# Performance work log

Measured on AMD Instinct MI355X. Metric: run time of the kernel, lower is better.

The kernel has to match this reference:

```python
import jax, jax.numpy as jnp
import numpy as np

STEP = 1  # spatial shift amount (module hard-codes narrow offset 1, so step=1)
EPS = 1e-5  # BatchNorm eps (torch default)


def conv1x1(x, W, b):
    # x: [B,C,H,W], W: [Co,C], b: [Co]
    return jnp.einsum('bchw,oc->bohw', x, W) + b[None, :, None, None]


def setup_inputs() -> dict:
    key = jax.random.key(0)
    ks = jax.random.split(key, 16)
    B, C, H, W = 32, 160, 112, 112
    Co = C // 5
    d = {}
    d['x'] = jax.random.normal(ks[0], (B, C, H, W), dtype=jnp.float32)
    # BatchNorm (inference-style) params
    d['gamma'] = jax.random.uniform(ks[1], (C,), minval=0.8, maxval=1.2)
    d['beta'] = jax.random.normal(ks[2], (C,)) * 0.05
    d['running_mean'] = jax.random.normal(ks[3], (C,)) * 0.1
    d['running_var'] = jax.random.uniform(ks[4], (C,), minval=0.5, maxval=1.5)
    # five 1x1 branch convs: weight [Co, C], bias [Co]
    names = ['t', 'b', 'r', 'l', 'c']
    for i, n in enumerate(names):
        d[f'W_{n}'] = jax.random.normal(ks[5 + i], (Co, C)) * 0.05
        d[f'b_{n}'] = jnp.zeros((Co,), dtype=jnp.float32)
    # final fuse conv: [C, C]
    d['W_fuse'] = jax.random.normal(ks[10], (C, C)) * 0.05
    d['b_fuse'] = jnp.zeros((C,), dtype=jnp.float32)
    return d


def reference(x, gamma, beta, running_mean, running_var,
              W_t, b_t, W_b, b_b, W_r, b_r, W_l, b_l, W_c, b_c,
              W_fuse, b_fuse):
    B, C, H, Wd = x.shape
    # BatchNorm2d (inference) + exact GELU (torch default)
    inv = gamma / jnp.sqrt(running_var + EPS)
    h = (x - running_mean[None, :, None, None]) * inv[None, :, None, None] + beta[None, :, None, None]
    h = jax.nn.gelu(h, approximate=False)
    # five parallel 1x1 projections, each C -> C//5
    xt = conv1x1(h, W_t, b_t)
    xb = conv1x1(h, W_b, b_b)
    xr = conv1x1(h, W_r, b_r)
    xl = conv1x1(h, W_l, b_l)
    xc = conv1x1(h, W_c, b_c)
    # spatial shifts: pad + narrow (torch F.pad order is (left,right,top,bottom))
    # x_t: pad bottom by STEP, take rows [1, 1+H)  -> shift up
    xt = jnp.pad(xt, ((0, 0), (0, 0), (0, STEP), (0, 0)))[:, :, 1:1 + H, :]
    # x_b: pad top by STEP, take rows [0, H)       -> shift down
    xb = jnp.pad(xb, ((0, 0), (0, 0), (STEP, 0), (0, 0)))[:, :, :H, :]
    # x_l: pad right by STEP, take cols [1, 1+W)   -> shift left
    xl = jnp.pad(xl, ((0, 0), (0, 0), (0, 0), (0, STEP)))[:, :, :, 1:1 + Wd]
    # x_r: pad left by STEP, take cols [0, W)      -> shift right
    xr = jnp.pad(xr, ((0, 0), (0, 0), (0, 0), (STEP, 0)))[:, :, :, :Wd]
    # concat in original order [t, b, r, l, c] then final 1x1 fuse
    cat = jnp.concatenate([xt, xb, xr, xl, xc], axis=1)  # [B, C, H, W]
    return conv1x1(cat, W_fuse, b_fuse)
```

## Files before the change

kernel.cpp:

```cpp
#include <hip/hip_runtime.h>
#include <hip/hip_bf16.h>

#define BATCH 32
#define C 160
#define H 112
#define W 112
#define HW (H * W)
#define NT 7
#define HP (H / 2)

typedef __bf16 bf16_t;
typedef bf16_t bf16x8 __attribute__((ext_vector_type(8)));
typedef float f32x4 __attribute__((ext_vector_type(4)));

#define P_BYTES   ((size_t)BATCH * C * HW * 2)
#define WALL_OFF  (P_BYTES)
#define WFRAG_B   (10 * 5 * 64 * 8 * 2)
#define WFUSE_OFF (WALL_OFF + WFRAG_B)
#define BN2_OFF   (WFUSE_OFF + WFRAG_B)
#define BALL_OFF  (BN2_OFF + C * 8)

__device__ __forceinline__ float gelu_exact(float h) {
    float u  = h * 0.70710678118654752f;
    float au = __builtin_fabsf(u);
    float tt = __builtin_amdgcn_rcpf(__builtin_fmaf(0.3275911f, au, 1.0f));
    float poly = tt * __builtin_fmaf(tt,
                      __builtin_fmaf(tt,
                      __builtin_fmaf(tt,
                      __builtin_fmaf(tt, 1.061405429f, -1.453152027f),
                                         1.421413741f),
                                        -0.284496736f),
                                         0.254829592f);
    float e  = __builtin_amdgcn_exp2f(-au * au * 1.4426950408889634f);
    float er = __builtin_fmaf(-poly, e, 1.0f);
    er = __builtin_copysignf(er, u);
    return 0.5f * h * (1.0f + er);
}

__global__ __launch_bounds__(256) void prep_kernel(
    const float* __restrict__ Wt, const float* __restrict__ Wb,
    const float* __restrict__ Wr, const float* __restrict__ Wl,
    const float* __restrict__ Wc,
    const float* __restrict__ bt, const float* __restrict__ bb,
    const float* __restrict__ br, const float* __restrict__ bl,
    const float* __restrict__ bc,
    const float* __restrict__ Wfuse,
    const float* __restrict__ gamma, const float* __restrict__ beta,
    const float* __restrict__ mean, const float* __restrict__ var,
    char* __restrict__ ws)
{
    bf16_t* wallf  = (bf16_t*)(ws + WALL_OFF);
    bf16_t* wfusef = (bf16_t*)(ws + WFUSE_OFF);
    float2* bn2 = (float2*)(ws + BN2_OFF);
    float*  ball = (float*)(ws + BALL_OFF);

    const float* Wbr[5] = {Wt, Wb, Wr, Wl, Wc};
    const float* bbr[5] = {bt, bb, br, bl, bc};

    int tid = blockIdx.x * blockDim.x + threadIdx.x;
    int nth = gridDim.x * blockDim.x;

    for (int idx = tid; idx < 10 * 5 * 64 * 8; idx += nth) {
        int j    = idx & 7;
        int lane = (idx >> 3) & 63;
        int rest = idx >> 9;
        int ks   = rest % 5;
        int mt   = rest / 5;
        int m  = mt * 16 + (lane & 15);
        int q  = lane >> 4;
        int k_nat = ks * 32 + q * 8 + j;
        wallf[idx] = (bf16_t)Wbr[m >> 5][(m & 31) * C + k_nat];
        int chan32 = (j < 4) ? (q * 4 + j) : (16 + q * 4 + (j - 4));
        wfusef[idx] = (bf16_t)Wfuse[m * C + ks * 32 + chan32];
    }
    for (int c = tid; c < C; c += nth) {
        float s = gamma[c] * rsqrtf(var[c] + 1e-5f);
        bn2[c] = make_float2(s, beta[c] - mean[c] * s);
        ball[c] = bbr[c >> 5][c & 31];
    }
}

__global__ __launch_bounds__(256, 2) void stage1_kernel(
    const float* __restrict__ x, char* __restrict__ ws)
{
    const bf16_t* __restrict__ wallf = (const bf16_t*)(ws + WALL_OFF);
    const float2* __restrict__ bn2 = (const float2*)(ws + BN2_OFF);
    const float*  __restrict__ ball = (const float*)(ws + BALL_OFF);
    bf16_t* __restrict__ P = (bf16_t*)ws;

    int wid  = blockIdx.x * 4 + (threadIdx.x >> 6);
    int lane = threadIdx.x & 63;
    int b   = wid / (HP * NT);
    int rem = wid - b * (HP * NT);
    int yp  = rem / NT;
    int t   = rem - yp * NT;
    int y0  = yp * 2;
    int nl = lane & 15, quad = lane >> 4;
    int px = t * 16 + nl;

    const float* xp = x + (size_t)b * C * HW + (size_t)y0 * W + px;

    float v0[40], v1[40];
#pragma unroll
    for (int i = 0; i < 40; ++i) {
        int ks = i >> 3, j = i & 7;
        size_t off = (size_t)(ks * 32 + quad * 8 + j) * HW;
        v0[i] = xp[off];
        v1[i] = xp[off + W];
    }
    __builtin_amdgcn_sched_barrier(0);

    f32x4 acc0[10], acc1[10];
#pragma unroll
    for (int mt = 0; mt < 10; ++mt) {
        f32x4 bias = *(const f32x4*)&ball[mt * 16 + quad * 4];
        acc0[mt] = bias;
        acc1[mt] = bias;
    }

#pragma unroll
    for (int ks = 0; ks < 5; ++ks) {
        bf16x8 bfrag0, bfrag1;
#pragma unroll
        for (int j = 0; j < 8; ++j) {
            int c = ks * 32 + quad * 8 + j;
            float2 sb = bn2[c];
            bfrag0[j] = (bf16_t)gelu_exact(__builtin_fmaf(v0[ks * 8 + j], sb.x, sb.y));
            bfrag1[j] = (bf16_t)gelu_exact(__builtin_fmaf(v1[ks * 8 + j], sb.x, sb.y));
        }
#pragma unroll
        for (int mt = 0; mt < 10; ++mt) {
            bf16x8 afrag = *(const bf16x8*)&wallf[((mt * 5 + ks) * 64 + lane) * 8];
            acc0[mt] = __builtin_amdgcn_mfma_f32_16x16x32_bf16(afrag, bfrag0, acc0[mt], 0, 0, 0);
            acc1[mt] = __builtin_amdgcn_mfma_f32_16x16x32_bf16(afrag, bfrag1, acc1[mt], 0, 0, 0);
        }
    }

    size_t pb = (((size_t)(b * 5) * H + y0) * W + px) * 32 + quad * 8;
#pragma unroll
    for (int kb = 0; kb < 5; ++kb) {
        bf16x8 o0, o1;
#pragma unroll
        for (int r = 0; r < 4; ++r) {
            o0[r]     = (bf16_t)acc0[kb * 2][r];
            o0[r + 4] = (bf16_t)acc0[kb * 2 + 1][r];
            o1[r]     = (bf16_t)acc1[kb * 2][r];
            o1[r + 4] = (bf16_t)acc1[kb * 2 + 1][r];
        }
        *(bf16x8*)&P[pb + (size_t)kb * HW * 32] = o0;
        *(bf16x8*)&P[pb + (size_t)kb * HW * 32 + (size_t)W * 32] = o1;
    }
}

__global__ __launch_bounds__(256, 2) void stage2_kernel(
    char* __restrict__ ws, const float* __restrict__ bfuse,
    float* __restrict__ out)
{
    const bf16_t* __restrict__ wfusef = (const bf16_t*)(ws + WFUSE_OFF);
    const bf16_t* __restrict__ P = (const bf16_t*)ws;

    int wid  = blockIdx.x * 4 + (threadIdx.x >> 6);
    int lane = threadIdx.x & 63;
    int b   = wid / (HP * NT);
    int rem = wid - b * (HP * NT);
    int yp  = rem / NT;
    int t   = rem - yp * NT;
    int y0  = yp * 2, y1 = y0 + 1;
    int nl = lane & 15, quad = lane >> 4;
    int px = t * 16 + nl;

    bf16x8 zero;
#pragma unroll
    for (int j = 0; j < 8; ++j) zero[j] = (bf16_t)0.0f;

    auto ldP = [&](int kb, int yy, int xx) -> bf16x8 {
        return *(const bf16x8*)&P[(((size_t)(b * 5 + kb) * H + yy) * W + xx) * 32 + quad * 8];
    };

    bf16x8 f0[5], f1[5];
    f0[0] = ldP(0, y0 + 1, px);
    f0[1] = ldP(1, y0 - 1 < 0 ? 0 : y0 - 1, px);
    f0[2] = ldP(2, y0, px == 0 ? 0 : px - 1);
    f0[3] = ldP(3, y0, px == W - 1 ? px : px + 1);
    f0[4] = ldP(4, y0, px);
    f1[0] = ldP(0, y1 + 1 >= H ? y1 : y1 + 1, px);
    f1[1] = ldP(1, y1 - 1, px);
    f1[2] = ldP(2, y1, px == 0 ? 0 : px - 1);
    f1[3] = ldP(3, y1, px == W - 1 ? px : px + 1);
    f1[4] = ldP(4, y1, px);
    __builtin_amdgcn_sched_barrier(0);

    if (y0 == 0)     f0[1] = zero;
    if (y1 + 1 >= H) f1[0] = zero;
    if (px == 0)     { f0[2] = zero; f1[2] = zero; }
    if (px == W - 1) { f0[3] = zero; f1[3] = zero; }

    f32x4 acc0[10], acc1[10];
#pragma unroll
    for (int mt = 0; mt < 10; ++mt) {
        f32x4 bias = *(const f32x4*)&bfuse[mt * 16 + quad * 4];
        acc0[mt] = bias;
        acc1[mt] = bias;
    }

#pragma unroll
    for (int ks = 0; ks < 5; ++ks) {
#pragma unroll
        for (int mt = 0; mt < 10; ++mt) {
            bf16x8 afrag = *(const bf16x8*)&wfusef[((mt * 5 + ks) * 64 + lane) * 8];
            acc0[mt] = __builtin_amdgcn_mfma_f32_16x16x32_bf16(afrag, f0[ks], acc0[mt], 0, 0, 0);
            acc1[mt] = __builtin_amdgcn_mfma_f32_16x16x32_bf16(afrag, f1[ks], acc1[mt], 0, 0, 0);
        }
    }

    size_t ob = (size_t)b * C * HW + (size_t)y0 * W + px;
#pragma unroll
    for (int mt = 0; mt < 10; ++mt) {
#pragma unroll
        for (int r = 0; r < 4; ++r) {
            int m = mt * 16 + quad * 4 + r;
            out[ob + (size_t)m * HW] = acc0[mt][r];
            out[ob + (size_t)m * HW + W] = acc1[mt][r];
        }
    }
}

extern "C" void kernel_launch(void* const* d_in, const int* in_sizes, int n_in,
                              void* d_out, int out_size, void* d_ws, size_t ws_size,
                              hipStream_t stream)
{
    const float* x     = (const float*)d_in[0];
    const float* gamma = (const float*)d_in[1];
    const float* beta  = (const float*)d_in[2];
    const float* mean  = (const float*)d_in[3];
    const float* var   = (const float*)d_in[4];
    const float* Wt    = (const float*)d_in[5];
    const float* bt    = (const float*)d_in[6];
    const float* Wb    = (const float*)d_in[7];
    const float* bb    = (const float*)d_in[8];
    const float* Wr    = (const float*)d_in[9];
    const float* br    = (const float*)d_in[10];
    const float* Wl    = (const float*)d_in[11];
    const float* bl    = (const float*)d_in[12];
    const float* Wc    = (const float*)d_in[13];
    const float* bc    = (const float*)d_in[14];
    const float* Wfuse = (const float*)d_in[15];
    const float* bfuse = (const float*)d_in[16];

    char* ws = (char*)d_ws;
    float* out = (float*)d_out;

    prep_kernel<<<64, 256, 0, stream>>>(Wt, Wb, Wr, Wl, Wc, bt, bb, br, bl, bc,
                                        Wfuse, gamma, beta, mean, var, ws);

    int nblocks = (BATCH * HP * NT) / 4;
    stage1_kernel<<<nblocks, 256, 0, stream>>>(x, ws);
    stage2_kernel<<<nblocks, 256, 0, stream>>>(ws, bfuse, out);
}
```

Before: 590.1 us.

## Fold branch convs into fuse weights and apply shifts on GELU activations

New measurement: 928.8 us. 57.4% more time.

```diff
diff --git a/kernel.cpp b/kernel.cpp
--- a/kernel.cpp
+++ b/kernel.cpp
@@ -13,12 +13,12 @@
 typedef bf16_t bf16x8 __attribute__((ext_vector_type(8)));
 typedef float f32x4 __attribute__((ext_vector_type(4)));
 
-#define P_BYTES   ((size_t)BATCH * C * HW * 2)
-#define WALL_OFF  (P_BYTES)
-#define WFRAG_B   (10 * 5 * 64 * 8 * 2)
-#define WFUSE_OFF (WALL_OFF + WFRAG_B)
-#define BN2_OFF   (WFUSE_OFF + WFRAG_B)
-#define BALL_OFF  (BN2_OFF + C * 8)
+#define H_BYTES   ((size_t)BATCH * HW * C * 2)
+#define WTAP_OFF  (H_BYTES)
+#define WTAP_B    (5 * C * C * 2)
+#define BTOT_OFF  (WTAP_OFF + WTAP_B)
+#define BIASK_OFF (BTOT_OFF + 640)
+#define BN2_OFF   (BIASK_OFF + 3200)
 
 __device__ __forceinline__ float gelu_exact(float h) {
     float u  = h * 0.70710678118654752f;
@@ -44,15 +44,15 @@
     const float* __restrict__ bt, const float* __restrict__ bb,
     const float* __restrict__ br, const float* __restrict__ bl,
     const float* __restrict__ bc,
-    const float* __restrict__ Wfuse,
+    const float* __restrict__ Wfuse, const float* __restrict__ bfuse,
     const float* __restrict__ gamma, const float* __restrict__ beta,
     const float* __restrict__ mean, const float* __restrict__ var,
     char* __restrict__ ws)
 {
-    bf16_t* wallf  = (bf16_t*)(ws + WALL_OFF);
-    bf16_t* wfusef = (bf16_t*)(ws + WFUSE_OFF);
-    float2* bn2 = (float2*)(ws + BN2_OFF);
-    float*  ball = (float*)(ws + BALL_OFF);
+    bf16_t* wtapf = (bf16_t*)(ws + WTAP_OFF);
+    float*  btot  = (float*)(ws + BTOT_OFF);
+    float*  biask = (float*)(ws + BIASK_OFF);
+    float2* bn2   = (float2*)(ws + BN2_OFF);
 
     const float* Wbr[5] = {Wt, Wb, Wr, Wl, Wc};
     const float* bbr[5] = {bt, bb, br, bl, bc};
@@ -60,104 +60,83 @@
     int tid = blockIdx.x * blockDim.x + threadIdx.x;
     int nth = gridDim.x * blockDim.x;
 
-    for (int idx = tid; idx < 10 * 5 * 64 * 8; idx += nth) {
+    for (int idx = tid; idx < 5 * 10 * 5 * 64 * 8; idx += nth) {
         int j    = idx & 7;
         int lane = (idx >> 3) & 63;
         int rest = idx >> 9;
-        int ks   = rest % 5;
-        int mt   = rest / 5;
-        int m  = mt * 16 + (lane & 15);
-        int q  = lane >> 4;
-        int k_nat = ks * 32 + q * 8 + j;
-        wallf[idx] = (bf16_t)Wbr[m >> 5][(m & 31) * C + k_nat];
-        int chan32 = (j < 4) ? (q * 4 + j) : (16 + q * 4 + (j - 4));
-        wfusef[idx] = (bf16_t)Wfuse[m * C + ks * 32 + chan32];
+        int kb   = rest % 5;
+        int tmp  = rest / 5;
+        int ks   = tmp % 5;
+        int mt   = tmp / 5;
+        int m = mt * 16 + (lane & 15);
+        int k = ks * 32 + (lane >> 4) * 8 + j;
+        float s = 0.0f;
+        const float* wf = Wfuse + m * C + kb * 32;
+        const float* wb2 = Wbr[kb];
+#pragma unroll 8
+        for (int o = 0; o < 32; ++o)
+            s = __builtin_fmaf(wf[o], wb2[o * C + k], s);
+        wtapf[idx] = (bf16_t)s;
     }
     for (int c = tid; c < C; c += nth) {
-        float s = gamma[c] * rsqrtf(var[c] + 1e-5f);
-        bn2[c] = make_float2(s, beta[c] - mean[c] * s);
-        ball[c] = bbr[c >> 5][c & 31];
-    }
-}
-
-__global__ __launch_bounds__(256, 2) void stage1_kernel(
+        float tot = bfuse[c];
+        for (int kb = 0; kb < 5; ++kb) {
+            float s = 0.0f;
+            const float* wf = Wfuse + c * C + kb * 32;
+            for (int o = 0; o < 32; ++o)
+                s = __builtin_fmaf(wf[o], bbr[kb][o], s);
+            biask[kb * C + c] = s;
+            tot += s;
+        }
+        btot[c] = tot;
+        float sc = gamma[c] * rsqrtf(var[c] + 1e-5f);
+        bn2[c] = make_float2(sc, beta[c] - mean[c] * sc);
+    }
+}
+
+__global__ __launch_bounds__(256) void stageh_kernel(
     const float* __restrict__ x, char* __restrict__ ws)
 {
-    const bf16_t* __restrict__ wallf = (const bf16_t*)(ws + WALL_OFF);
     const float2* __restrict__ bn2 = (const float2*)(ws + BN2_OFF);
-    const float*  __restrict__ ball = (const float*)(ws + BALL_OFF);
-    bf16_t* __restrict__ P = (bf16_t*)ws;
-
-    int wid  = blockIdx.x * 4 + (threadIdx.x >> 6);
-    int lane = threadIdx.x & 63;
-    int b   = wid / (HP * NT);
-    int rem = wid - b * (HP * NT);
-    int yp  = rem / NT;
-    int t   = rem - yp * NT;
-    int y0  = yp * 2;
-    int nl = lane & 15, quad = lane >> 4;
-    int px = t * 16 + nl;
-
-    const float* xp = x + (size_t)b * C * HW + (size_t)y0 * W + px;
-
-    float v0[40], v1[40];
-#pragma unroll
-    for (int i = 0; i < 40; ++i) {
-        int ks = i >> 3, j = i & 7;
-        size_t off = (size_t)(ks * 32 + quad * 8 + j) * HW;
-        v0[i] = xp[off];
-        v1[i] = xp[off + W];
-    }
-    __builtin_amdgcn_sched_barrier(0);
-
-    f32x4 acc0[10], acc1[10];
-#pragma unroll
-    for (int mt = 0; mt < 10; ++mt) {
-        f32x4 bias = *(const f32x4*)&ball[mt * 16 + quad * 4];
-        acc0[mt] = bias;
-        acc1[mt] = bias;
-    }
-
-#pragma unroll
-    for (int ks = 0; ks < 5; ++ks) {
-        bf16x8 bfrag0, bfrag1;
-#pragma unroll
-        for (int j = 0; j < 8; ++j) {
-            int c = ks * 32 + quad * 8 + j;
-            float2 sb = bn2[c];
-            bfrag0[j] = (bf16_t)gelu_exact(__builtin_fmaf(v0[ks * 8 + j], sb.x, sb.y));
-            bfrag1[j] = (bf16_t)gelu_exact(__builtin_fmaf(v1[ks * 8 + j], sb.x, sb.y));
-        }
-#pragma unroll
-        for (int mt = 0; mt < 10; ++mt) {
-            bf16x8 afrag = *(const bf16x8*)&wallf[((mt * 5 + ks) * 64 + lane) * 8];
-            acc0[mt] = __builtin_amdgcn_mfma_f32_16x16x32_bf16(afrag, bfrag0, acc0[mt], 0, 0, 0);
-            acc1[mt] = __builtin_amdgcn_mfma_f32_16x16x32_bf16(afrag, bfrag1, acc1[mt], 0, 0, 0);
-        }
-    }
-
-    size_t pb = (((size_t)(b * 5) * H + y0) * W + px) * 32 + quad * 8;
-#pragma unroll
-    for (int kb = 0; kb < 5; ++kb) {
-        bf16x8 o0, o1;
-#pragma unroll
-        for (int r = 0; r < 4; ++r) {
-            o0[r]     = (bf16_t)acc0[kb * 2][r];
-            o0[r + 4] = (bf16_t)acc0[kb * 2 + 1][r];
-            o1[r]     = (bf16_t)acc1[kb * 2][r];
-            o1[r + 4] = (bf16_t)acc1[kb * 2 + 1][r];
-        }
-        *(bf16x8*)&P[pb + (size_t)kb * HW * 32] = o0;
-        *(bf16x8*)&P[pb + (size_t)kb * HW * 32 + (size_t)W * 32] = o1;
-    }
-}
-
-__global__ __launch_bounds__(256, 2) void stage2_kernel(
-    char* __restrict__ ws, const float* __restrict__ bfuse,
-    float* __restrict__ out)
-{
-    const bf16_t* __restrict__ wfusef = (const bf16_t*)(ws + WFUSE_OFF);
-    const bf16_t* __restrict__ P = (const bf16_t*)ws;
+    bf16_t* __restrict__ h = (bf16_t*)ws;
+
+    int tid = blockIdx.x * 256 + threadIdx.x;
+    int x2  = tid % 56;
+    int y   = (tid / 56) % H;
+    int c32 = (tid / (56 * H)) % 5;
+    int b   = tid / (56 * H * 5);
+    int px  = x2 * 2;
+
+    const float* xp = x + ((size_t)b * C + c32 * 32) * HW + y * W + px;
+
+    float2 v[32];
+#pragma unroll
+    for (int j = 0; j < 32; ++j)
+        v[j] = *(const float2*)(xp + (size_t)j * HW);
+
+    bf16x8 o0[4], o1[4];
+#pragma unroll
+    for (int j = 0; j < 32; ++j) {
+        float2 sb = bn2[c32 * 32 + j];
+        o0[j >> 3][j & 7] = (bf16_t)gelu_exact(__builtin_fmaf(v[j].x, sb.x, sb.y));
+        o1[j >> 3][j & 7] = (bf16_t)gelu_exact(__builtin_fmaf(v[j].y, sb.x, sb.y));
+    }
+
+    bf16_t* hp = h + ((size_t)b * HW + (size_t)y * W + px) * C + c32 * 32;
+#pragma unroll
+    for (int k = 0; k < 4; ++k) {
+        *(bf16x8*)(hp + k * 8) = o0[k];
+        *(bf16x8*)(hp + C + k * 8) = o1[k];
+    }
+}
+
+__global__ __launch_bounds__(256, 2) void stagef_kernel(
+    char* __restrict__ ws, float* __restrict__ out)
+{
+    const bf16_t* __restrict__ h = (const bf16_t*)ws;
+    const bf16_t* __restrict__ wtapf = (const bf16_t*)(ws + WTAP_OFF);
+    const float*  __restrict__ btot  = (const float*)(ws + BTOT_OFF);
+    const float*  __restrict__ biask = (const float*)(ws + BIASK_OFF);
 
     int wid  = blockIdx.x * 4 + (threadIdx.x >> 6);
     int lane = threadIdx.x & 63;
@@ -169,47 +148,91 @@
     int nl = lane & 15, quad = lane >> 4;
     int px = t * 16 + nl;
 
-    bf16x8 zero;
-#pragma unroll
-    for (int j = 0; j < 8; ++j) zero[j] = (bf16_t)0.0f;
-
-    auto ldP = [&](int kb, int yy, int xx) -> bf16x8 {
-        return *(const bf16x8*)&P[(((size_t)(b * 5 + kb) * H + yy) * W + xx) * 32 + quad * 8];
-    };
-
-    bf16x8 f0[5], f1[5];
-    f0[0] = ldP(0, y0 + 1, px);
-    f0[1] = ldP(1, y0 - 1 < 0 ? 0 : y0 - 1, px);
-    f0[2] = ldP(2, y0, px == 0 ? 0 : px - 1);
-    f0[3] = ldP(3, y0, px == W - 1 ? px : px + 1);
-    f0[4] = ldP(4, y0, px);
-    f1[0] = ldP(0, y1 + 1 >= H ? y1 : y1 + 1, px);
-    f1[1] = ldP(1, y1 - 1, px);
-    f1[2] = ldP(2, y1, px == 0 ? 0 : px - 1);
-    f1[3] = ldP(3, y1, px == W - 1 ? px : px + 1);
-    f1[4] = ldP(4, y1, px);
-    __builtin_amdgcn_sched_barrier(0);
-
-    if (y0 == 0)     f0[1] = zero;
-    if (y1 + 1 >= H) f1[0] = zero;
-    if (px == 0)     { f0[2] = zero; f1[2] = zero; }
-    if (px == W - 1) { f0[3] = zero; f1[3] = zero; }
+    bool m_up = (y0 == 0);
+    bool m_dn = (y1 == H - 1);
+    bool m_l  = (px == 0);
+    bool m_r  = (px == W - 1);
+    int ym  = m_up ? 0 : y0 - 1;
+    int ypl = m_dn ? y1 : y1 + 1;
+    int pxl = m_l ? px : px - 1;
+    int pxr = m_r ? px : px + 1;
+
+    const bf16_t* hb = h + (size_t)b * HW * C;
 
     f32x4 acc0[10], acc1[10];
 #pragma unroll
     for (int mt = 0; mt < 10; ++mt) {
-        f32x4 bias = *(const f32x4*)&bfuse[mt * 16 + quad * 4];
+        f32x4 bias = *(const f32x4*)&btot[mt * 16 + quad * 4];
         acc0[mt] = bias;
         acc1[mt] = bias;
     }
 
+    bf16x8 zero;
+#pragma unroll
+    for (int j = 0; j < 8; ++j) zero[j] = (bf16_t)0.0f;
+
 #pragma unroll
     for (int ks = 0; ks < 5; ++ks) {
+        int co = ks * 32 + quad * 8;
+        auto ldh = [&](int yy, int xx) -> bf16x8 {
+            return *(const bf16x8*)&hb[((size_t)yy * W + xx) * C + co];
+        };
+        bf16x8 S0 = ldh(ym, px);
+        bf16x8 S1 = ldh(y0, px);
+        bf16x8 S2 = ldh(y1, px);
+        bf16x8 S3 = ldh(ypl, px);
+        bf16x8 L0 = ldh(y0, pxl);
+        bf16x8 L1 = ldh(y1, pxl);
+        bf16x8 R0 = ldh(y0, pxr);
+        bf16x8 R1 = ldh(y1, pxr);
+        if (m_up) S0 = zero;
+        if (m_dn) S3 = zero;
+        if (m_l) { L0 = zero; L1 = zero; }
+        if (m_r) { R0 = zero; R1 = zero; }
+
 #pragma unroll
         for (int mt = 0; mt < 10; ++mt) {
-            bf16x8 afrag = *(const bf16x8*)&wfusef[((mt * 5 + ks) * 64 + lane) * 8];
-            acc0[mt] = __builtin_amdgcn_mfma_f32_16x16x32_bf16(afrag, f0[ks], acc0[mt], 0, 0, 0);
-            acc1[mt] = __builtin_amdgcn_mfma_f32_16x16x32_bf16(afrag, f1[ks], acc1[mt], 0, 0, 0);
+            const bf16_t* wp = &wtapf[(size_t)(((mt * 5 + ks) * 5) * 64 + lane) * 8];
+            bf16x8 a_t = *(const bf16x8*)(wp + 0 * 512);
+            bf16x8 a_b = *(const bf16x8*)(wp + 1 * 512);
+            bf16x8 a_r = *(const bf16x8*)(wp + 2 * 512);
+            bf16x8 a_l = *(const bf16x8*)(wp + 3 * 512);
+            bf16x8 a_c = *(const bf16x8*)(wp + 4 * 512);
+            acc0[mt] = __builtin_amdgcn_mfma_f32_16x16x32_bf16(a_t, S2, acc0[mt], 0, 0, 0);
+            acc1[mt] = __builtin_amdgcn_mfma_f32_16x16x32_bf16(a_t, S3, acc1[mt], 0, 0, 0);
+            acc0[mt] = __builtin_amdgcn_mfma_f32_16x16x32_bf16(a_b, S0, acc0[mt], 0, 0, 0);
+            acc1[mt] = __builtin_amdgcn_mfma_f32_16x16x32_bf16(a_b, S1, acc1[mt], 0, 0, 0);
+            acc0[mt] = __builtin_amdgcn_mfma_f32_16x16x32_bf16(a_r, L0, acc0[mt], 0, 0, 0);
+            acc1[mt] = __builtin_amdgcn_mfma_f32_16x16x32_bf16(a_r, L1, acc1[mt], 0, 0, 0);
+            acc0[mt] = __builtin_amdgcn_mfma_f32_16x16x32_bf16(a_l, R0, acc0[mt], 0, 0, 0);
+            acc1[mt] = __builtin_amdgcn_mfma_f32_16x16x32_bf16(a_l, R1, acc1[mt], 0, 0, 0);
+            acc0[mt] = __builtin_amdgcn_mfma_f32_16x16x32_bf16(a_c, S1, acc0[mt], 0, 0, 0);
+            acc1[mt] = __builtin_amdgcn_mfma_f32_16x16x32_bf16(a_c, S2, acc1[mt], 0, 0, 0);
+        }
+    }
+
+    if (y0 == 0) {
+#pragma unroll
+        for (int mt = 0; mt < 10; ++mt)
+            acc0[mt] -= *(const f32x4*)&biask[1 * C + mt * 16 + quad * 4];
+    }
+    if (y1 == H - 1) {
+#pragma unroll
+        for (int mt = 0; mt < 10; ++mt)
+            acc1[mt] -= *(const f32x4*)&biask[0 * C + mt * 16 + quad * 4];
+    }
+    if (m_l) {
+#pragma unroll
+        for (int mt = 0; mt < 10; ++mt) {
+            f32x4 c2 = *(const f32x4*)&biask[2 * C + mt * 16 + quad * 4];
+            acc0[mt] -= c2; acc1[mt] -= c2;
+        }
+    }
+    if (m_r) {
+#pragma unroll
+        for (int mt = 0; mt < 10; ++mt) {
+            f32x4 c2 = *(const f32x4*)&biask[3 * C + mt * 16 + quad * 4];
+            acc0[mt] -= c2; acc1[mt] -= c2;
         }
     }
 
@@ -250,10 +273,12 @@
     char* ws = (char*)d_ws;
     float* out = (float*)d_out;
 
-    prep_kernel<<<64, 256, 0, stream>>>(Wt, Wb, Wr, Wl, Wc, bt, bb, br, bl, bc,
-                                        Wfuse, gamma, beta, mean, var, ws);
-
-    int nblocks = (BATCH * HP * NT) / 4;
-    stage1_kernel<<<nblocks, 256, 0, stream>>>(x, ws);
-    stage2_kernel<<<nblocks, 256, 0, stream>>>(ws, bfuse, out);
-}
+    prep_kernel<<<160, 256, 0, stream>>>(Wt, Wb, Wr, Wl, Wc, bt, bb, br, bl, bc,
+                                         Wfuse, bfuse, gamma, beta, mean, var, ws);
+
+    int nh = (BATCH * 5 * H * 56) / 256;
+    stageh_kernel<<<nh, 256, 0, stream>>>(x, ws);
+
+    int nf = (BATCH * HP * NT) / 4;
+    stagef_kernel<<<nf, 256, 0, stream>>>(ws, out);
+}
```
